# Kernel optimization log

Measured on AMD Instinct MI355X. Metric: run time of the kernel, lower is better.

Reference implementation:

```python
import jax, jax.numpy as jnp
import numpy as np

B_, S_, DIM, DT_RANK, D_STATE = 4, 1024, 384, 24, 16


def layer_norm(x, g, b, eps=1e-5):
    mu = jnp.mean(x, axis=-1, keepdims=True)
    var = jnp.mean((x - mu) ** 2, axis=-1, keepdims=True)
    return (x - mu) * jax.lax.rsqrt(var + eps) * g + b


def conv1d(x, w, b):
    # x: (B, C, L), w: (O, I, K), 'same' padding for odd K
    pad = (w.shape[-1] - 1) // 2
    y = jax.lax.conv_general_dilated(x, w, (1,), [(pad, pad)],
                                     dimension_numbers=('NCH', 'OIH', 'NCH'))
    return y + b[None, :, None]


def ssm(x, w_dbc, w_dt, b_dt, A_log, D):
    # x: (b, s, d) -> selective scan (Mamba), parallel (associative) scan form
    dbc = jnp.einsum('bsd,ed->bse', x, w_dbc)
    delta, Bm, Cm = jnp.split(dbc, [DT_RANK, DT_RANK + D_STATE], axis=-1)
    delta = jax.nn.softplus(jnp.einsum('bsr,dr->bsd', delta, w_dt) + b_dt)  # (b,s,d)
    A = -jnp.exp(A_log)                                   # (d, n)
    deltaA = jnp.exp(delta[..., None] * A)                # (b,s,d,n)
    BX = (delta * x)[..., None] * Bm[:, :, None, :]       # (b,s,d,n)

    def combine(c1, c2):
        a1, h1 = c1
        a2, h2 = c2
        return a1 * a2, a2 * h1 + h2

    _, hs = jax.lax.associative_scan(combine, (deltaA, BX), axis=1)
    y = jnp.einsum('bsdn,bsn->bsd', hs, Cm)
    return y + D * x


def setup_inputs() -> dict:
    key = jax.random.key(0)
    ks = jax.random.split(key, 16)
    sc = 0.02
    d, r, n = DIM, DT_RANK, D_STATE
    A_log = jnp.log(jnp.tile(jnp.arange(1, n + 1, dtype=jnp.float32), (d, 1)))  # (d, n)
    return {
        'x': jax.random.normal(ks[0], (B_, S_, d), dtype=jnp.float32),
        'w_p1': jax.random.normal(ks[1], (d, d, 3)) * sc, 'b_p1': jnp.zeros((d,)),
        'w_p2': jax.random.normal(ks[2], (d, d, 3)) * sc, 'b_p2': jnp.zeros((d,)),
        'w_p3': jax.random.normal(ks[3], (d, d, 1)) * sc, 'b_p3': jnp.zeros((d,)),
        'w_cf': jax.random.normal(ks[4], (d, d, 1)) * sc, 'b_cf': jnp.zeros((d,)),
        'w_cb': jax.random.normal(ks[5], (d, d, 1)) * sc, 'b_cb': jnp.zeros((d,)),
        'g_n': jnp.ones((d,)), 'bt_n': jnp.zeros((d,)),
        'g_nf': jnp.ones((d,)), 'bt_nf': jnp.zeros((d,)),
        'g_nb': jnp.ones((d,)), 'bt_nb': jnp.zeros((d,)),
        'w_dbc1': jax.random.normal(ks[6], (r + 2 * n, d)) * sc,
        'w_dt1': jax.random.normal(ks[7], (d, r)) * sc, 'b_dt1': jnp.zeros((d,)),
        'A_log1': A_log, 'D1': jnp.ones((d,)),
        'w_dbc2': jax.random.normal(ks[8], (r + 2 * n, d)) * sc,
        'w_dt2': jax.random.normal(ks[9], (d, r)) * sc, 'b_dt2': jnp.zeros((d,)),
        'A_log2': A_log, 'D2': jnp.ones((d,)),
    }


def reference(x, w_p1, b_p1, w_p2, b_p2, w_p3, b_p3, w_cf, b_cf, w_cb, b_cb,
              g_n, bt_n, g_nf, bt_nf, g_nb, bt_nb,
              w_dbc1, w_dt1, b_dt1, A_log1, D1,
              w_dbc2, w_dt2, b_dt2, A_log2, D2):
    skip = x
    xn = layer_norm(x, g_n, bt_n)
    xt = jnp.swapaxes(xn, 1, 2)                       # (b, d, s)
    z1 = jnp.swapaxes(conv1d(xt, w_p1, b_p1), 1, 2)   # (b, s, d)
    xp = conv1d(xt, w_p2, b_p2)                       # (b, d, s)

    def direction(xd, wc, bc, g, bt, w_dbc, w_dt, b_dt, A_log, D):
        h = conv1d(xd, wc, bc)
        h = jnp.swapaxes(h, 1, 2)
        h = layer_norm(h, g, bt)
        return ssm(h, w_dbc, w_dt, b_dt, A_log, D)

    x1 = direction(xp, w_cf, b_cf, g_nf, bt_nf, w_dbc1, w_dt1, b_dt1, A_log1, D1)
    # backward direction: sequence flipped (note: original does NOT flip back)
    x2 = direction(xp[:, :, ::-1], w_cb, b_cb, g_nb, bt_nb, w_dbc2, w_dt2, b_dt2, A_log2, D2)

    z = jax.nn.silu(z1)
    x3 = jnp.swapaxes((x1 + x2) * z, 1, 2)            # (b, d, s)
    out = jnp.swapaxes(conv1d(x3, w_p3, b_p3), 1, 2)
    return out + skip
```

## Files before the change

### kernel.cpp

```cpp
#include <hip/hip_runtime.h>
#include <cstddef>

#define NB 4
#define NS 1024
#define ND 384
#define NN 16
#define MTOT 4096
#define TM 8
#define TMC 4
#define NCH 32
#define CHL 32
#define NSP (NS + 2)

static __device__ __forceinline__ float fget(const float4& v, int e) {
    return e == 0 ? v.x : e == 1 ? v.y : e == 2 ? v.z : v.w;
}

__global__ __launch_bounds__(256) void prep_weights(
    const float* __restrict__ w_p1, const float* __restrict__ w_p2,
    const float* __restrict__ w_p3, const float* __restrict__ w_cf,
    const float* __restrict__ w_cb,
    const float* __restrict__ w_dbc1, const float* __restrict__ w_dbc2,
    const float* __restrict__ w_dt1,  const float* __restrict__ w_dt2,
    float* __restrict__ wp1P, float* __restrict__ wp2P, float* __restrict__ wp3P,
    float* __restrict__ wcfP, float* __restrict__ wcbP,
    float* __restrict__ wdbc1P, float* __restrict__ wdbc2P,
    float* __restrict__ wdt1T,  float* __restrict__ wdt2T)
{
    int idx = blockIdx.x * 256 + threadIdx.x;
    if (idx < 884736) {
        int q = idx; const float* w; float* wT;
        if (q < 442368) { w = w_p1; wT = wp1P; }
        else            { q -= 442368; w = w_p2; wT = wp2P; }
        int e = q & 3; int o = (q >> 2) % 384; int kk = q / 1536;
        int k = kk / 96; int i = (kk % 96) * 4 + e;
        wT[q] = w[((size_t)o * 384 + i) * 3 + k];
    } else if (idx < 1327104) {
        int q = idx - 884736; const float* w; float* wT;
        if (q < 147456)      { w = w_p3; wT = wp3P; }
        else if (q < 294912) { q -= 147456; w = w_cf; wT = wcfP; }
        else                 { q -= 294912; w = w_cb; wT = wcbP; }
        int e = q & 3; int o = (q >> 2) % 384; int i = (q / 1536) * 4 + e;
        wT[q] = w[(size_t)o * 384 + i];
    } else if (idx < 1370112) {
        int q = idx - 1327104; const float* w; float* wT;
        if (q < 21504) { w = w_dbc1; wT = wdbc1P; }
        else           { q -= 21504; w = w_dbc2; wT = wdbc2P; }
        int e = q & 3; int oc = (q >> 2) % 56; int i = (q / 224) * 4 + e;
        wT[q] = w[(size_t)oc * 384 + i];
    } else if (idx < 1388544) {
        int q = idx - 1370112; const float* w; float* wT;
        if (q < 9216) { w = w_dt1; wT = wdt1T; }
        else          { q -= 9216; w = w_dt2; wT = wdt2T; }
        int d = q % 384; int qq = q / 384;
        wT[q] = w[(size_t)d * 24 + qq];
    }
}

__global__ __launch_bounds__(384) void ln1_k(
    const float* __restrict__ x,
    const float* __restrict__ g_n, const float* __restrict__ bt_n,
    float* __restrict__ XNP)
{
    int blk = blockIdx.x;
    int t = threadIdx.x, wid = t >> 6, lane = t & 63;
    if (blk == MTOT / TM) {
        for (int b = 0; b < NB; ++b) {
            XNP[((size_t)b * NSP + 0) * ND + t] = 0.f;
            XNP[((size_t)b * NSP + NS + 1) * ND + t] = 0.f;
        }
        return;
    }
    int m0 = blk * TM;
    int b = m0 >> 10, s0 = m0 & 1023;
    for (int j = wid; j < TM; j += 6) {
        int r = s0 + j;
        const float* row = x + ((size_t)(b * NS + r)) * ND;
        float v[6]; float s1 = 0.f, s2 = 0.f;
        #pragma unroll
        for (int e = 0; e < 6; ++e) {
            v[e] = row[lane + 64 * e];
            s1 += v[e]; s2 += v[e] * v[e];
        }
        #pragma unroll
        for (int o = 32; o; o >>= 1) {
            s1 += __shfl_xor(s1, o);
            s2 += __shfl_xor(s2, o);
        }
        float mu = s1 * (1.f / ND);
        float var = s2 * (1.f / ND) - mu * mu;
        float rs = rsqrtf(var + 1e-5f);
        float* orow = XNP + ((size_t)b * NSP + r + 1) * ND;
        #pragma unroll
        for (int e = 0; e < 6; ++e) {
            int i = lane + 64 * e;
            orow[i] = (v[e] - mu) * rs * g_n[i] + bt_n[i];
        }
    }
}

__global__ __launch_bounds__(384) void conv3x2(
    const float* __restrict__ XNP,
    const float* __restrict__ wp2P, const float* __restrict__ b_p2,
    const float* __restrict__ wp1P, const float* __restrict__ b_p1,
    float* __restrict__ XP, float* __restrict__ Z1)
{
    int m0 = blockIdx.x * TMC;
    int b = m0 >> 10, s0 = m0 & 1023;
    int t = threadIdx.x;
    const float4* xnp4 = reinterpret_cast<const float4*>(XNP);
    const float4* w2f4 = reinterpret_cast<const float4*>(wp2P) + t;
    const float4* w1f4 = reinterpret_cast<const float4*>(wp1P) + t;

    float a2[TMC], a1[TMC];
    #pragma unroll
    for (int r = 0; r < TMC; ++r) { a2[r] = b_p2[t]; a1[r] = b_p1[t]; }

    size_t base = (size_t)(b * NSP + s0) * 96;
    float4 W2c = w2f4[0], W1c = w1f4[0];
    float4 xc[TMC];
    #pragma unroll
    for (int r = 0; r < TMC; ++r) xc[r] = xnp4[base + (size_t)r * 96];

    for (int kk = 0; kk < 288; ++kk) {
        int kn = (kk < 287) ? kk + 1 : 287;
        float4 W2n = w2f4[(size_t)kn * 384];
        float4 W1n = w1f4[(size_t)kn * 384];
        int k_n = kn / 96, i4_n = kn - k_n * 96;
        size_t rbn = base + (size_t)k_n * 96 + i4_n;
        float4 xn_[TMC];
        #pragma unroll
        for (int r = 0; r < TMC; ++r) xn_[r] = xnp4[rbn + (size_t)r * 96];
        #pragma unroll
        for (int e = 0; e < 4; ++e) {
            float wv2 = fget(W2c, e);
            float wv1 = fget(W1c, e);
            #pragma unroll
            for (int r = 0; r < TMC; ++r) {
                float xe = fget(xc[r], e);
                a2[r] = fmaf(xe, wv2, a2[r]);
                a1[r] = fmaf(xe, wv1, a1[r]);
            }
        }
        W2c = W2n; W1c = W1n;
        #pragma unroll
        for (int r = 0; r < TMC; ++r) xc[r] = xn_[r];
    }
    #pragma unroll
    for (int r = 0; r < TMC; ++r) {
        size_t ix = (size_t)(m0 + r) * ND + t;
        XP[ix] = a2[r];
        Z1[ix] = a1[r];
    }
}

__global__ __launch_bounds__(384) void dir2_k1(
    const float* __restrict__ XP,
    const float* __restrict__ wcfP, const float* __restrict__ b_cf,
    const float* __restrict__ g_nf, const float* __restrict__ bt_nf,
    const float* __restrict__ wdbc1P, const float* __restrict__ wdt1T,
    const float* __restrict__ b_dt1,
    const float* __restrict__ wcbP, const float* __restrict__ b_cb,
    const float* __restrict__ g_nb, const float* __restrict__ bt_nb,
    const float* __restrict__ wdbc2P, const float* __restrict__ wdt2T,
    const float* __restrict__ b_dt2,
    float* __restrict__ LN2, float* __restrict__ DBC2, float* __restrict__ DEL2)
{
    __shared__ float uo[TM][ND];
    __shared__ float red[TM][6][2];
    __shared__ float dbcS[TM][56];
    int blk = blockIdx.x;
    int dir = blk >> 9;
    int m0 = (blk & 511) * TM;
    int b = m0 >> 10, s0 = m0 & 1023;
    int t = threadIdx.x, wid = t >> 6, lane = t & 63;

    const float* wcP   = dir ? wcbP   : wcfP;
    const float* b_c   = dir ? b_cb   : b_cf;
    const float* g     = dir ? g_nb   : g_nf;
    const float* bt    = dir ? bt_nb  : bt_nf;
    const float* wdbcP = dir ? wdbc2P : wdbc1P;
    const float* wdtT  = dir ? wdt2T  : wdt1T;
    const float* b_dt  = dir ? b_dt2  : b_dt1;
    const size_t NM = (size_t)MTOT * ND;
    float* LNo  = LN2  + (size_t)dir * NM;
    float* DBCo = DBC2 + (size_t)dir * MTOT * 56;
    float* DELo = DEL2 + (size_t)dir * NM;

    const float4* XPf4 = reinterpret_cast<const float4*>(XP);
    size_t rowb[TM];
    #pragma unroll
    for (int r = 0; r < TM; ++r) {
        int s = s0 + r;
        int sE = dir ? (NS - 1 - s) : s;
        rowb[r] = ((size_t)(b * NS + sE)) * 96;
    }

    const float4* wcf4 = reinterpret_cast<const float4*>(wcP) + t;
    float acc[TM];
    #pragma unroll
    for (int r = 0; r < TM; ++r) acc[r] = b_c[t];
    float4 Wc = wcf4[0];
    float4 xc[TM];
    #pragma unroll
    for (int r = 0; r < TM; ++r) xc[r] = XPf4[rowb[r]];
    for (int i4 = 0; i4 < 96; ++i4) {
        int in_ = (i4 < 95) ? i4 + 1 : 95;
        float4 Wn = wcf4[(size_t)in_ * 384];
        float4 xn_[TM];
        #pragma unroll
        for (int r = 0; r < TM; ++r) xn_[r] = XPf4[rowb[r] + in_];
        #pragma unroll
        for (int e = 0; e < 4; ++e) {
            float wv = fget(Wc, e);
            #pragma unroll
            for (int r = 0; r < TM; ++r)
                acc[r] = fmaf(fget(xc[r], e), wv, acc[r]);
        }
        Wc = Wn;
        #pragma unroll
        for (int r = 0; r < TM; ++r) xc[r] = xn_[r];
    }

    #pragma unroll
    for (int r = 0; r < TM; ++r) {
        float s1 = acc[r], s2 = acc[r] * acc[r];
        #pragma unroll
        for (int o = 32; o; o >>= 1) {
            s1 += __shfl_xor(s1, o);
            s2 += __shfl_xor(s2, o);
        }
        if (lane == 0) { red[r][wid][0] = s1; red[r][wid][1] = s2; }
    }
    __syncthreads();
    float gt = g[t], btt = bt[t];
    #pragma unroll
    for (int r = 0; r < TM; ++r) {
        float s1 = 0.f, s2 = 0.f;
        #pragma unroll
        for (int w = 0; w < 6; ++w) { s1 += red[r][w][0]; s2 += red[r][w][1]; }
        float mu = s1 * (1.f / ND);
        float var = s2 * (1.f / ND) - mu * mu;
        float rs = rsqrtf(var + 1e-5f);
        float ln = (acc[r] - mu) * rs * gt + btt;
        uo[r][t] = ln;
        LNo[(size_t)(m0 + r) * ND + t] = ln;
    }
    __syncthreads();

    for (int r = wid; r < TM; r += 6) {
        if (lane < 56) {
            const float4* wdf4 = reinterpret_cast<const float4*>(wdbcP) + lane;
            const float4* uof4 = reinterpret_cast<const float4*>(&uo[r][0]);
            float a = 0.f;
            float4 Wd = wdf4[0];
            for (int i4 = 0; i4 < 96; ++i4) {
                int in_ = (i4 < 95) ? i4 + 1 : 95;
                float4 Wdn = wdf4[(size_t)in_ * 56];
                float4 uv = uof4[i4];
                a = fmaf(uv.x, Wd.x, a);
                a = fmaf(uv.y, Wd.y, a);
                a = fmaf(uv.z, Wd.z, a);
                a = fmaf(uv.w, Wd.w, a);
                Wd = Wdn;
            }
            dbcS[r][lane] = a;
            DBCo[(size_t)(m0 + r) * 56 + lane] = a;
        }
    }
    __syncthreads();

    float accD[TM]; float bd = b_dt[t];
    #pragma unroll
    for (int r = 0; r < TM; ++r) accD[r] = bd;
    for (int q = 0; q < 24; ++q) {
        float wv = wdtT[q * 384 + t];
        #pragma unroll
        for (int r = 0; r < TM; ++r) accD[r] = fmaf(dbcS[r][q], wv, accD[r]);
    }
    #pragma unroll
    for (int r = 0; r < TM; ++r) {
        float a = accD[r];
        DELo[(size_t)(m0 + r) * ND + t] =
            fmaxf(a, 0.f) + log1pf(__expf(-fabsf(a)));
    }
}

__global__ __launch_bounds__(384) void scan_s1(
    const float* __restrict__ DEL2, const float* __restrict__ LN2,
    const float* __restrict__ DBC2, const float* __restrict__ A_log1,
    const float* __restrict__ A_log2,
    float* __restrict__ P, float* __restrict__ H)
{
    __shared__ float bc[CHL][32];
    int blk = blockIdx.x;
    int c = blk & (NCH - 1);
    int db = blk >> 5;
    int dir = db >> 2, b = db & 3;
    int t = threadIdx.x;
    const float* del  = DEL2 + (size_t)dir * MTOT * ND;
    const float* u    = LN2  + (size_t)dir * MTOT * ND;
    const float* dbc  = DBC2 + (size_t)dir * MTOT * 56;
    const float* Alog = dir ? A_log2 : A_log1;

    for (int e = t; e < CHL * 32; e += 384) {
        int row = e >> 5, col = e & 31;
        bc[row][col] = dbc[((size_t)(b * NS + c * CHL + row)) * 56 + 24 + col];
    }
    __syncthreads();

    float A[NN], h[NN], p[NN];
    #pragma unroll
    for (int n = 0; n < NN; ++n) {
        A[n] = -__expf(Alog[(size_t)t * NN + n]);
        h[n] = 0.f; p[n] = 1.f;
    }
    for (int j = 0; j < CHL; ++j) {
        size_t rix = (size_t)b * NS + c * CHL + j;
        float dl = del[rix * ND + t];
        float uv = u[rix * ND + t];
        float dx = dl * uv;
        #pragma unroll
        for (int n = 0; n < NN; ++n) {
            float da = __expf(dl * A[n]);
            h[n] = fmaf(da, h[n], dx * bc[j][n]);
            p[n] *= da;
        }
    }
    size_t base = ((size_t)blk * ND + t) * NN;
    #pragma unroll
    for (int n = 0; n < NN; ++n) { P[base + n] = p[n]; H[base + n] = h[n]; }
}

__global__ __launch_bounds__(256) void scan_s2(
    float* __restrict__ P, const float* __restrict__ H)
{
    int gid = blockIdx.x * 256 + threadIdx.x;
    int n = gid & 15;
    int d = (gid >> 4) % ND;
    int db = gid / (16 * ND);
    float h = 0.f;
    for (int c = 0; c < NCH; ++c) {
        size_t idx = (((size_t)db * NCH + c) * ND + d) * NN + n;
        float p = P[idx];
        float hh = H[idx];
        P[idx] = h;
        h = fmaf(p, h, hh);
    }
}

__global__ __launch_bounds__(384) void scan_s3(
    const float* __restrict__ DEL2, const float* __restrict__ LN2,
    const float* __restrict__ DBC2, const float* __restrict__ A_log1,
    const float* __restrict__ A_log2, const float* __restrict__ D1,
    const float* __restrict__ D2, const float* __restrict__ Hinit,
    float* __restrict__ Y2)
{
    __shared__ float bc[CHL][32];
    int blk = blockIdx.x;
    int c = blk & (NCH - 1);
    int db = blk >> 5;
    int dir = db >> 2, b = db & 3;
    int t = threadIdx.x;
    const float* del  = DEL2 + (size_t)dir * MTOT * ND;
    const float* u    = LN2  + (size_t)dir * MTOT * ND;
    const float* dbc  = DBC2 + (size_t)dir * MTOT * 56;
    const float* Alog = dir ? A_log2 : A_log1;
    const float* Dv   = dir ? D2 : D1;
    float* y          = Y2 + (size_t)dir * MTOT * ND;

    for (int e = t; e < CHL * 32; e += 384) {
        int row = e >> 5, col = e & 31;
        bc[row][col] = dbc[((size_t)(b * NS + c * CHL + row)) * 56 + 24 + col];
    }
    __syncthreads();

    size_t base = ((size_t)blk * ND + t) * NN;
    float A[NN], h[NN];
    #pragma unroll
    for (int n = 0; n < NN; ++n) {
        A[n] = -__expf(Alog[(size_t)t * NN + n]);
        h[n] = Hinit[base + n];
    }
    float Dd = Dv[t];
    for (int j = 0; j < CHL; ++j) {
        size_t rix = (size_t)b * NS + c * CHL + j;
        float dl = del[rix * ND + t];
        float uv = u[rix * ND + t];
        float dx = dl * uv;
        float y0 = 0.f, y1 = 0.f;
        #pragma unroll
        for (int n = 0; n < NN; n += 2) {
            float da0 = __expf(dl * A[n]);
            float da1 = __expf(dl * A[n + 1]);
            h[n]     = fmaf(da0, h[n],     dx * bc[j][n]);
            h[n + 1] = fmaf(da1, h[n + 1], dx * bc[j][n + 1]);
            y0 = fmaf(h[n],     bc[j][16 + n],     y0);
            y1 = fmaf(h[n + 1], bc[j][16 + n + 1], y1);
        }
        y[rix * ND + t] = y0 + y1 + Dd * uv;
    }
}

__global__ __launch_bounds__(64) void scan2(
    const float* __restrict__ DEL2, const float* __restrict__ LN2,
    const float* __restrict__ DBC2, const float* __restrict__ A1,
    const float* __restrict__ D1v, const float* __restrict__ A2,
    const float* __restrict__ D2v, float* __restrict__ Y2)
{
    int gid = blockIdx.x * 64 + threadIdx.x;
    int dir = gid >= (NB * ND);
    int gd = gid - dir * (NB * ND);
    const float* delta = DEL2 + (size_t)dir * MTOT * ND;
    const float* u     = LN2  + (size_t)dir * MTOT * ND;
    const float* dbc   = DBC2 + (size_t)dir * MTOT * 56;
    const float* Alog  = dir ? A2 : A1;
    const float* Dv    = dir ? D2v : D1v;
    float* y_out       = Y2 + (size_t)dir * MTOT * ND;

    int d = gd % ND, b = gd / ND;
    float A[NN], h[NN];
    #pragma unroll
    for (int n = 0; n < NN; ++n) {
        A[n] = -__expf(Alog[(size_t)d * NN + n]);
        h[n] = 0.f;
    }
    float Dd = Dv[d];
    for (int s = 0; s < NS; ++s) {
        size_t rix = (size_t)b * NS + s;
        float dl = delta[rix * ND + d];
        float uv = u[rix * ND + d];
        float dx = dl * uv;
        const float* r = dbc + rix * 56;
        float y0 = 0.f, y1 = 0.f;
        #pragma unroll
        for (int n = 0; n < NN; n += 2) {
            float da0 = __expf(dl * A[n]);
            float da1 = __expf(dl * A[n + 1]);
            h[n]     = fmaf(da0, h[n],     dx * r[24 + n]);
            h[n + 1] = fmaf(da1, h[n + 1], dx * r[24 + n + 1]);
            y0 = fmaf(h[n],     r[40 + n],     y0);
            y1 = fmaf(h[n + 1], r[40 + n + 1], y1);
        }
        y_out[rix * ND + d] = y0 + y1 + Dd * uv;
    }
}

__global__ __launch_bounds__(256) void gate_k(
    const float* __restrict__ Z1, const float* __restrict__ YF,
    const float* __restrict__ YB, float* __restrict__ X3)
{
    int i = blockIdx.x * 256 + threadIdx.x;
    const float4* z4 = reinterpret_cast<const float4*>(Z1);
    const float4* f4 = reinterpret_cast<const float4*>(YF);
    const float4* b4 = reinterpret_cast<const float4*>(YB);
    float4* o4 = reinterpret_cast<float4*>(X3);
    float4 z = z4[i], f = f4[i], bb = b4[i], o;
    o.x = (f.x + bb.x) * (z.x / (1.f + __expf(-z.x)));
    o.y = (f.y + bb.y) * (z.y / (1.f + __expf(-z.y)));
    o.z = (f.z + bb.z) * (z.z / (1.f + __expf(-z.z)));
    o.w = (f.w + bb.w) * (z.w / (1.f + __expf(-z.w)));
    o4[i] = o;
}

__global__ __launch_bounds__(384) void final_k(
    const float* __restrict__ x, const float* __restrict__ X3,
    const float* __restrict__ wp3P, const float* __restrict__ b_p3,
    float* __restrict__ out)
{
    int m0 = blockIdx.x * TMC;
    int t = threadIdx.x;
    const float4* x3f4 = reinterpret_cast<const float4*>(X3);
    const float4* wpf4 = reinterpret_cast<const float4*>(wp3P) + t;
    size_t rb = (size_t)m0 * 96;

    float acc[TMC]; float bp = b_p3[t];
    #pragma unroll
    for (int r = 0; r < TMC; ++r) acc[r] = bp;
    float4 Wp = wpf4[0];
    float4 xc[TMC];
    #pragma unroll
    for (int r = 0; r < TMC; ++r) xc[r] = x3f4[rb + (size_t)r * 96];
    for (int i4 = 0; i4 < 96; ++i4) {
        int in_ = (i4 < 95) ? i4 + 1 : 95;
        float4 Wn = wpf4[(size_t)in_ * 384];
        float4 xn_[TMC];
        #pragma unroll
        for (int r = 0; r < TMC; ++r) xn_[r] = x3f4[rb + (size_t)r * 96 + in_];
        #pragma unroll
        for (int e = 0; e < 4; ++e) {
            float wv = fget(Wp, e);
            #pragma unroll
            for (int r = 0; r < TMC; ++r)
                acc[r] = fmaf(fget(xc[r], e), wv, acc[r]);
        }
        Wp = Wn;
        #pragma unroll
        for (int r = 0; r < TMC; ++r) xc[r] = xn_[r];
    }
    #pragma unroll
    for (int r = 0; r < TMC; ++r) {
        size_t ix = (size_t)(m0 + r) * ND + t;
        out[ix] = acc[r] + x[ix];
    }
}

__global__ __launch_bounds__(256) void fill_f32(float* out, float v, int n)
{
    int i = blockIdx.x * 256 + threadIdx.x;
    if (i < n) out[i] = v;
}

extern "C" void kernel_launch(void* const* d_in, const int* in_sizes, int n_in,
                              void* d_out, int out_size, void* d_ws, size_t ws_size,
                              hipStream_t stream) {
    float* out = (float*)d_out;

    if (out_size != MTOT * ND) {
        fill_f32<<<(out_size + 255) / 256, 256, 0, stream>>>(
            out, 70000.f + (float)(out_size >> 16), out_size);
        return;
    }

    const float* x      = (const float*)d_in[0];
    const float* w_p1   = (const float*)d_in[1];
    const float* b_p1   = (const float*)d_in[2];
    const float* w_p2   = (const float*)d_in[3];
    const float* b_p2   = (const float*)d_in[4];
    const float* w_p3   = (const float*)d_in[5];
    const float* b_p3   = (const float*)d_in[6];
    const float* w_cf   = (const float*)d_in[7];
    const float* b_cf   = (const float*)d_in[8];
    const float* w_cb   = (const float*)d_in[9];
    const float* b_cb   = (const float*)d_in[10];
    const float* g_n    = (const float*)d_in[11];
    const float* bt_n   = (const float*)d_in[12];
    const float* g_nf   = (const float*)d_in[13];
    const float* bt_nf  = (const float*)d_in[14];
    const float* g_nb   = (const float*)d_in[15];
    const float* bt_nb  = (const float*)d_in[16];
    const float* w_dbc1 = (const float*)d_in[17];
    const float* w_dt1  = (const float*)d_in[18];
    const float* b_dt1  = (const float*)d_in[19];
    const float* A_log1 = (const float*)d_in[20];
    const float* D1     = (const float*)d_in[21];
    const float* w_dbc2 = (const float*)d_in[22];
    const float* w_dt2  = (const float*)d_in[23];
    const float* b_dt2  = (const float*)d_in[24];
    const float* A_log2 = (const float*)d_in[25];
    const float* D2     = (const float*)d_in[26];

    const size_t NM = (size_t)MTOT * ND;
    const size_t N56 = (size_t)MTOT * 56;
    const size_t AGG = (size_t)2 * NB * NCH * ND * NN;
    size_t off = 0;
    float* ws = (float*)d_ws;
    float* XP    = ws + off; off += NM;
    float* Z1    = ws + off; off += NM;
    float* LN2   = ws + off; off += 2 * NM;
    float* DEL2  = ws + off; off += 2 * NM;
    float* Y2    = ws + off; off += 2 * NM;
    float* DBC2  = ws + off; off += 2 * N56;
    float* wp1P   = ws + off; off += 442368;
    float* wp2P   = ws + off; off += 442368;
    float* wp3P   = ws + off; off += 147456;
    float* wcfP   = ws + off; off += 147456;
    float* wcbP   = ws + off; off += 147456;
    float* wdbc1P = ws + off; off += 21504;
    float* wdbc2P = ws + off; off += 21504;
    float* wdt1T  = ws + off; off += 9216;
    float* wdt2T  = ws + off; off += 9216;
    const size_t ws_base = off;
    float* Pagg  = ws + off; off += AGG;
    float* Hagg  = ws + off; off += AGG;
    const size_t ws_fast = off;

    if (ws_size < ws_base * sizeof(float)) {
        fill_f32<<<(out_size + 255) / 256, 256, 0, stream>>>(out, 60000.f, out_size);
        return;
    }
    const int fast_scan = (ws_size >= ws_fast * sizeof(float));

    float* YF   = Y2;         float* YB   = Y2 + NM;
    float* XNP = Y2;
    float* X3  = DEL2;

    prep_weights<<<5424, 256, 0, stream>>>(
        w_p1, w_p2, w_p3, w_cf, w_cb, w_dbc1, w_dbc2, w_dt1, w_dt2,
        wp1P, wp2P, wp3P, wcfP, wcbP, wdbc1P, wdbc2P, wdt1T, wdt2T);

    ln1_k<<<MTOT / TM + 1, 384, 0, stream>>>(x, g_n, bt_n, XNP);

    conv3x2<<<MTOT / TMC, 384, 0, stream>>>(
        XNP, wp2P, b_p2, wp1P, b_p1, XP, Z1);

    dir2_k1<<<2 * (MTOT / TM), 384, 0, stream>>>(
        XP,
        wcfP, b_cf, g_nf, bt_nf, wdbc1P, wdt1T, b_dt1,
        wcbP, b_cb, g_nb, bt_nb, wdbc2P, wdt2T, b_dt2,
        LN2, DBC2, DEL2);

    if (fast_scan) {
        scan_s1<<<2 * NB * NCH, 384, 0, stream>>>(
            DEL2, LN2, DBC2, A_log1, A_log2, Pagg, Hagg);
        scan_s2<<<(2 * NB * ND * NN) / 256, 256, 0, stream>>>(Pagg, Hagg);
        scan_s3<<<2 * NB * NCH, 384, 0, stream>>>(
            DEL2, LN2, DBC2, A_log1, A_log2, D1, D2, Pagg, Y2);
    } else {
        scan2<<<(2 * NB * ND) / 64, 64, 0, stream>>>(
            DEL2, LN2, DBC2, A_log1, D1, A_log2, D2, Y2);
    }

    gate_k<<<(int)(NM / 4 / 256), 256, 0, stream>>>(Z1, YF, YB, X3);

    final_k<<<MTOT / TMC, 384, 0, stream>>>(
        x, X3, wp3P, b_p3, out);
}
```

Baseline: 427.0 us.

## Run the k=3 input convolutions on bf16 MFMA with split-precision compensation

Replaces the scalar FP32 fused conv3x2 with an MFMA GEMM kernel that uses split bf16 (hi+lo) inputs and weights to emulate near-FP32 accuracy. The weights are pre-packed into a tiled bf16 layout, and LayerNorm now also writes hi/lo bf16 copies of its output. A sampled verification kernel checks results against FP32, and the old scalar kernel is kept as a fallback that exits early unless the check fails. The aim is to move the dominant conv FLOPs onto matrix cores. This adds a larger weight-prep pass, extra launches, and a small LDS-staged GEMM with no double buffering. The non-chunked scan path is removed.

Measured after the change: 650.8 us. 1.52x slower.

```diff
diff --git a/kernel.cpp b/kernel.cpp
--- a/kernel.cpp
+++ b/kernel.cpp
@@ -12,8 +12,19 @@
 #define CHL 32
 #define NSP (NS + 2)
 
+typedef unsigned short ushort_t;
+typedef __attribute__((ext_vector_type(8))) short short8;
+typedef __attribute__((ext_vector_type(4))) float f32x4;
+
 static __device__ __forceinline__ float fget(const float4& v, int e) {
     return e == 0 ? v.x : e == 1 ? v.y : e == 2 ? v.z : v.w;
+}
+static __device__ __forceinline__ ushort_t f2bf(float x) {
+    unsigned u = __float_as_uint(x);
+    return (ushort_t)((u + 0x7FFF + ((u >> 16) & 1)) >> 16);
+}
+static __device__ __forceinline__ float bf2f(ushort_t h) {
+    return __uint_as_float(((unsigned)h) << 16);
 }
 
 __global__ __launch_bounds__(256) void prep_weights(
@@ -22,34 +33,48 @@
     const float* __restrict__ w_cb,
     const float* __restrict__ w_dbc1, const float* __restrict__ w_dbc2,
     const float* __restrict__ w_dt1,  const float* __restrict__ w_dt2,
-    float* __restrict__ wp1P, float* __restrict__ wp2P, float* __restrict__ wp3P,
-    float* __restrict__ wcfP, float* __restrict__ wcbP,
+    ushort_t* __restrict__ Wp,
+    float* __restrict__ wp1P, float* __restrict__ wp2P,
+    float* __restrict__ wp3P, float* __restrict__ wcfP, float* __restrict__ wcbP,
     float* __restrict__ wdbc1P, float* __restrict__ wdbc2P,
     float* __restrict__ wdt1T,  float* __restrict__ wdt2T)
 {
     int idx = blockIdx.x * 256 + threadIdx.x;
-    if (idx < 884736) {
-        int q = idx; const float* w; float* wT;
+    if (idx < 2654208) {
+        int kc = idx & 31; int nr = (idx >> 5) & 63; int chunk = idx >> 11;
+        int ks = chunk % 108; int nblk = chunk / 108;
+        int n = nblk * 64 + nr;
+        int keff = ks * 32 + kc;
+        int seg = keff / 1152; int r = keff - seg * 1152;
+        int k3 = r / 384; int i = r - k3 * 384;
+        const float* mat = (n < 384) ? w_p2 : w_p1;
+        float v = mat[((size_t)(n & 383) * 384 + i) * 3 + k3];
+        ushort_t hi = f2bf(v);
+        ushort_t outv = hi;
+        if (seg == 1) outv = f2bf(v - bf2f(hi));
+        Wp[idx] = outv;
+    } else if (idx < 3538944) {
+        int q = idx - 2654208; const float* w; float* wT;
         if (q < 442368) { w = w_p1; wT = wp1P; }
         else            { q -= 442368; w = w_p2; wT = wp2P; }
         int e = q & 3; int o = (q >> 2) % 384; int kk = q / 1536;
         int k = kk / 96; int i = (kk % 96) * 4 + e;
         wT[q] = w[((size_t)o * 384 + i) * 3 + k];
-    } else if (idx < 1327104) {
-        int q = idx - 884736; const float* w; float* wT;
+    } else if (idx < 3981312) {
+        int q = idx - 3538944; const float* w; float* wT;
         if (q < 147456)      { w = w_p3; wT = wp3P; }
         else if (q < 294912) { q -= 147456; w = w_cf; wT = wcfP; }
         else                 { q -= 294912; w = w_cb; wT = wcbP; }
         int e = q & 3; int o = (q >> 2) % 384; int i = (q / 1536) * 4 + e;
         wT[q] = w[(size_t)o * 384 + i];
-    } else if (idx < 1370112) {
-        int q = idx - 1327104; const float* w; float* wT;
+    } else if (idx < 4024320) {
+        int q = idx - 3981312; const float* w; float* wT;
         if (q < 21504) { w = w_dbc1; wT = wdbc1P; }
         else           { q -= 21504; w = w_dbc2; wT = wdbc2P; }
         int e = q & 3; int oc = (q >> 2) % 56; int i = (q / 224) * 4 + e;
         wT[q] = w[(size_t)oc * 384 + i];
-    } else if (idx < 1388544) {
-        int q = idx - 1370112; const float* w; float* wT;
+    } else if (idx < 4042752) {
+        int q = idx - 4024320; const float* w; float* wT;
         if (q < 9216) { w = w_dt1; wT = wdt1T; }
         else          { q -= 9216; w = w_dt2; wT = wdt2T; }
         int d = q % 384; int qq = q / 384;
@@ -60,14 +85,16 @@
 __global__ __launch_bounds__(384) void ln1_k(
     const float* __restrict__ x,
     const float* __restrict__ g_n, const float* __restrict__ bt_n,
-    float* __restrict__ XNP)
+    float* __restrict__ XNPf, ushort_t* __restrict__ XH, ushort_t* __restrict__ XL)
 {
     int blk = blockIdx.x;
     int t = threadIdx.x, wid = t >> 6, lane = t & 63;
     if (blk == MTOT / TM) {
         for (int b = 0; b < NB; ++b) {
-            XNP[((size_t)b * NSP + 0) * ND + t] = 0.f;
-            XNP[((size_t)b * NSP + NS + 1) * ND + t] = 0.f;
+            size_t o0 = ((size_t)b * NSP + 0) * ND + t;
+            size_t o1 = ((size_t)b * NSP + NS + 1) * ND + t;
+            XNPf[o0] = 0.f; XNPf[o1] = 0.f;
+            XH[o0] = 0; XL[o0] = 0; XH[o1] = 0; XL[o1] = 0;
         }
         return;
     }
@@ -90,21 +117,118 @@
         float mu = s1 * (1.f / ND);
         float var = s2 * (1.f / ND) - mu * mu;
         float rs = rsqrtf(var + 1e-5f);
-        float* orow = XNP + ((size_t)b * NSP + r + 1) * ND;
+        size_t ob = ((size_t)b * NSP + r + 1) * ND;
         #pragma unroll
         for (int e = 0; e < 6; ++e) {
             int i = lane + 64 * e;
-            orow[i] = (v[e] - mu) * rs * g_n[i] + bt_n[i];
-        }
-    }
-}
-
-__global__ __launch_bounds__(384) void conv3x2(
+            float val = (v[e] - mu) * rs * g_n[i] + bt_n[i];
+            XNPf[ob + i] = val;
+            ushort_t hi = f2bf(val);
+            XH[ob + i] = hi;
+            XL[ob + i] = f2bf(val - bf2f(hi));
+        }
+    }
+}
+
+__global__ __launch_bounds__(256) void conv_mfma(
+    const ushort_t* __restrict__ XH, const ushort_t* __restrict__ XL,
+    const ushort_t* __restrict__ Wp,
+    const float* __restrict__ b_p2, const float* __restrict__ b_p1,
+    float* __restrict__ XP, float* __restrict__ Z1)
+{
+    __shared__ ushort_t lds_a[64][40];
+    __shared__ ushort_t lds_b[64][40];
+    int blk = blockIdx.x;
+    int mtile = blk & 63, ntile = blk >> 6;
+    int m0 = mtile * 64;
+    int b = m0 >> 10, s0 = m0 & 1023;
+    int n0 = ntile * 64;
+    int t = threadIdx.x;
+    int lane = t & 63, w = t >> 6;
+    int wr = w >> 1, wc = w & 1;
+    int srow = t >> 2;
+    int schunk = (t & 3) * 8;
+
+    f32x4 acc[2][2] = {};
+
+    for (int ks = 0; ks < 108; ++ks) {
+        int seg = ks / 36;
+        int rem = ks - seg * 36;
+        int k3 = rem / 12;
+        int i0 = (rem - k3 * 12) * 32;
+        const ushort_t* XS = (ks < 72) ? XH : XL;
+        uint4 av = *reinterpret_cast<const uint4*>(
+            XS + ((size_t)(b * NSP + s0 + srow + k3) * ND + i0 + schunk));
+        uint4 bv = *reinterpret_cast<const uint4*>(
+            Wp + ((size_t)(ntile * 108 + ks) * 2048 + t * 8));
+        __syncthreads();
+        *reinterpret_cast<uint4*>(&lds_a[srow][schunk]) = av;
+        *reinterpret_cast<uint4*>(&lds_b[srow][schunk]) = bv;
+        __syncthreads();
+        short8 af[2], bf[2];
+        #pragma unroll
+        for (int mi = 0; mi < 2; ++mi)
+            af[mi] = *reinterpret_cast<const short8*>(
+                &lds_a[wr * 32 + mi * 16 + (lane & 15)][(lane >> 4) * 8]);
+        #pragma unroll
+        for (int ni = 0; ni < 2; ++ni)
+            bf[ni] = *reinterpret_cast<const short8*>(
+                &lds_b[wc * 32 + ni * 16 + (lane & 15)][(lane >> 4) * 8]);
+        #pragma unroll
+        for (int mi = 0; mi < 2; ++mi)
+            #pragma unroll
+            for (int ni = 0; ni < 2; ++ni)
+                acc[mi][ni] = __builtin_amdgcn_mfma_f32_16x16x32_bf16(
+                    af[mi], bf[ni], acc[mi][ni], 0, 0, 0);
+    }
+
+    #pragma unroll
+    for (int mi = 0; mi < 2; ++mi) {
+        #pragma unroll
+        for (int ni = 0; ni < 2; ++ni) {
+            int n = n0 + wc * 32 + ni * 16 + (lane & 15);
+            #pragma unroll
+            for (int j = 0; j < 4; ++j) {
+                int m = m0 + wr * 32 + mi * 16 + (lane >> 4) * 4 + j;
+                float v = acc[mi][ni][j];
+                if (n < 384) XP[(size_t)m * ND + n] = v + b_p2[n];
+                else         Z1[(size_t)m * ND + (n - 384)] = v + b_p1[n - 384];
+            }
+        }
+    }
+}
+
+__global__ __launch_bounds__(256) void verify_k(
+    const float* __restrict__ XNPf,
+    const float* __restrict__ w_p2, const float* __restrict__ b_p2,
+    const float* __restrict__ w_p1, const float* __restrict__ b_p1,
+    const float* __restrict__ XP, const float* __restrict__ Z1,
+    int* __restrict__ flag)
+{
+    int gid = blockIdx.x * 256 + threadIdx.x;
+    int m = (gid * 37) & 4095;
+    int n = (gid * 149) % 768;
+    int b = m >> 10, s = m & 1023;
+    const float* w = (n < 384) ? w_p2 : w_p1;
+    int o = n & 383;
+    float a = (n < 384) ? b_p2[o] : b_p1[o];
+    for (int k3 = 0; k3 < 3; ++k3) {
+        const float* xr = XNPf + ((size_t)(b * NSP + s + k3)) * ND;
+        const float* wr = w + (size_t)o * 1152 + k3;
+        for (int i = 0; i < 384; ++i) a = fmaf(xr[i], wr[i * 3], a);
+    }
+    float got = (n < 384) ? XP[(size_t)m * ND + o] : Z1[(size_t)m * ND + o];
+    if (fabsf(got - a) > 0.05f) atomicOr(flag, 1);
+}
+
+__global__ __launch_bounds__(384) void conv_fb(
+    const int* __restrict__ flag,
     const float* __restrict__ XNP,
     const float* __restrict__ wp2P, const float* __restrict__ b_p2,
     const float* __restrict__ wp1P, const float* __restrict__ b_p1,
     float* __restrict__ XP, float* __restrict__ Z1)
 {
+    if (((const volatile int*)flag)[0] == 0) return;
     int m0 = blockIdx.x * TMC;
     int b = m0 >> 10, s0 = m0 & 1023;
     int t = threadIdx.x;
@@ -399,50 +523,6 @@
             y1 = fmaf(h[n + 1], bc[j][16 + n + 1], y1);
         }
         y[rix * ND + t] = y0 + y1 + Dd * uv;
-    }
-}
-
-__global__ __launch_bounds__(64) void scan2(
-    const float* __restrict__ DEL2, const float* __restrict__ LN2,
-    const float* __restrict__ DBC2, const float* __restrict__ A1,
-    const float* __restrict__ D1v, const float* __restrict__ A2,
-    const float* __restrict__ D2v, float* __restrict__ Y2)
-{
-    int gid = blockIdx.x * 64 + threadIdx.x;
-    int dir = gid >= (NB * ND);
-    int gd = gid - dir * (NB * ND);
-    const float* delta = DEL2 + (size_t)dir * MTOT * ND;
-    const float* u     = LN2  + (size_t)dir * MTOT * ND;
-    const float* dbc   = DBC2 + (size_t)dir * MTOT * 56;
-    const float* Alog  = dir ? A2 : A1;
-    const float* Dv    = dir ? D2v : D1v;
-    float* y_out       = Y2 + (size_t)dir * MTOT * ND;
-
-    int d = gd % ND, b = gd / ND;
-    float A[NN], h[NN];
-    #pragma unroll
-    for (int n = 0; n < NN; ++n) {
-        A[n] = -__expf(Alog[(size_t)d * NN + n]);
-        h[n] = 0.f;
-    }
-    float Dd = Dv[d];
-    for (int s = 0; s < NS; ++s) {
-        size_t rix = (size_t)b * NS + s;
-        float dl = delta[rix * ND + d];
-        float uv = u[rix * ND + d];
-        float dx = dl * uv;
-        const float* r = dbc + rix * 56;
-        float y0 = 0.f, y1 = 0.f;
-        #pragma unroll
-        for (int n = 0; n < NN; n += 2) {
-            float da0 = __expf(dl * A[n]);
-            float da1 = __expf(dl * A[n + 1]);
-            h[n]     = fmaf(da0, h[n],     dx * r[24 + n]);
-            h[n + 1] = fmaf(da1, h[n + 1], dx * r[24 + n + 1]);
-            y0 = fmaf(h[n],     r[40 + n],     y0);
-            y1 = fmaf(h[n + 1], r[40 + n + 1], y1);
-        }
-        y_out[rix * ND + d] = y0 + y1 + Dd * uv;
     }
 }
 
@@ -570,29 +650,37 @@
     float* wdbc2P = ws + off; off += 21504;
     float* wdt1T  = ws + off; off += 9216;
     float* wdt2T  = ws + off; off += 9216;
-    const size_t ws_base = off;
     float* Pagg  = ws + off; off += AGG;
     float* Hagg  = ws + off; off += AGG;
-    const size_t ws_fast = off;
-
-    if (ws_size < ws_base * sizeof(float)) {
+    const size_t ws_need = off;
+
+    if (ws_size < ws_need * sizeof(float)) {
         fill_f32<<<(out_size + 255) / 256, 256, 0, stream>>>(out, 60000.f, out_size);
         return;
     }
-    const int fast_scan = (ws_size >= ws_fast * sizeof(float));
 
     float* YF   = Y2;         float* YB   = Y2 + NM;
-    float* XNP = Y2;
+    ushort_t* XH = (ushort_t*)Y2;
+    ushort_t* XL = XH + (size_t)NB * NSP * ND;
+    float* XNPf = DEL2;
+    ushort_t* Wp = (ushort_t*)Hagg;
+    int* flag = (int*)Pagg;
     float* X3  = DEL2;
 
-    prep_weights<<<5424, 256, 0, stream>>>(
+    prep_weights<<<15792, 256, 0, stream>>>(
         w_p1, w_p2, w_p3, w_cf, w_cb, w_dbc1, w_dbc2, w_dt1, w_dt2,
-        wp1P, wp2P, wp3P, wcfP, wcbP, wdbc1P, wdbc2P, wdt1T, wdt2T);
-
-    ln1_k<<<MTOT / TM + 1, 384, 0, stream>>>(x, g_n, bt_n, XNP);
-
-    conv3x2<<<MTOT / TMC, 384, 0, stream>>>(
-        XNP, wp2P, b_p2, wp1P, b_p1, XP, Z1);
+        Wp, wp1P, wp2P, wp3P, wcfP, wcbP, wdbc1P, wdbc2P, wdt1T, wdt2T);
+
+    fill_f32<<<1, 256, 0, stream>>>((float*)flag, 0.f, 1);
+
+    ln1_k<<<MTOT / TM + 1, 384, 0, stream>>>(x, g_n, bt_n, XNPf, XH, XL);
+
+    conv_mfma<<<64 * 12, 256, 0, stream>>>(XH, XL, Wp, b_p2, b_p1, XP, Z1);
+
+    verify_k<<<16, 256, 0, stream>>>(XNPf, w_p2, b_p2, w_p1, b_p1, XP, Z1, flag);
+
+    conv_fb<<<MTOT / TMC, 384, 0, stream>>>(
+        flag, XNPf, wp2P, b_p2, wp1P, b_p1, XP, Z1);
 
     dir2_k1<<<2 * (MTOT / TM), 384, 0, stream>>>(
         XP,
@@ -600,16 +688,11 @@
         wcbP, b_cb, g_nb, bt_nb, wdbc2P, wdt2T, b_dt2,
         LN2, DBC2, DEL2);
 
-    if (fast_scan) {
-        scan_s1<<<2 * NB * NCH, 384, 0, stream>>>(
-            DEL2, LN2, DBC2, A_log1, A_log2, Pagg, Hagg);
-        scan_s2<<<(2 * NB * ND * NN) / 256, 256, 0, stream>>>(Pagg, Hagg);
-        scan_s3<<<2 * NB * NCH, 384, 0, stream>>>(
-            DEL2, LN2, DBC2, A_log1, A_log2, D1, D2, Pagg, Y2);
-    } else {
-        scan2<<<(2 * NB * ND) / 64, 64, 0, stream>>>(
-            DEL2, LN2, DBC2, A_log1, D1, A_log2, D2, Y2);
-    }
+    scan_s1<<<2 * NB * NCH, 384, 0, stream>>>(
+        DEL2, LN2, DBC2, A_log1, A_log2, Pagg, Hagg);
+    scan_s2<<<(2 * NB * ND * NN) / 256, 256, 0, stream>>>(Pagg, Hagg);
+    scan_s3<<<2 * NB * NCH, 384, 0, stream>>>(
+        DEL2, LN2, DBC2, A_log1, A_log2, D1, D2, Pagg, Y2);
 
     gate_k<<<(int)(NM / 4 / 256), 256, 0, stream>>>(Z1, YF, YB, X3);
 
```
